# Kernel optimization log

Measured on AMD Instinct MI355X. Metric: run time of the kernel, lower is better.

Reference implementation:

```python
import jax, jax.numpy as jnp
import numpy as np

IN_FEATURES = 1024
OUT_FEATURES = 64   # per-head dim
NUM_HEADS = 16
DIM_PER_HEAD = IN_FEATURES // NUM_HEADS  # used for the 1/sqrt scale, per original code
B, S = 4, 1024


def setup_inputs() -> dict:
    key = jax.random.key(0)
    ks = jax.random.split(key, 12)
    HD = NUM_HEADS * OUT_FEATURES
    s = 1.0 / np.sqrt(IN_FEATURES)
    inp = {
        "q": jax.random.normal(ks[0], (B, S, IN_FEATURES), jnp.float32),
        "k": jax.random.normal(ks[1], (B, S, IN_FEATURES), jnp.float32),
        "v": jax.random.normal(ks[2], (B, S, IN_FEATURES), jnp.float32),
        "q_mask": jax.random.randint(ks[3], (B, S, 1), 0, 2).astype(jnp.float32),
        "k_mask": jax.random.randint(ks[4], (B, S, 1), 0, 2).astype(jnp.float32),
        "Wq": jax.random.normal(ks[5], (IN_FEATURES, HD), jnp.float32) * s,
        "bq": jnp.zeros((HD,), jnp.float32),
        "Wk": jax.random.normal(ks[6], (IN_FEATURES, HD), jnp.float32) * s,
        "bk": jnp.zeros((HD,), jnp.float32),
        "Wv": jax.random.normal(ks[7], (IN_FEATURES, HD), jnp.float32) * s,
        "bv": jnp.zeros((HD,), jnp.float32),
        "Wf": jax.random.normal(ks[8], (HD, IN_FEATURES), jnp.float32) * s,
        "bf": jnp.zeros((IN_FEATURES,), jnp.float32),
        "gamma": jnp.ones((IN_FEATURES,), jnp.float32),
        "beta": jnp.zeros((IN_FEATURES,), jnp.float32),
    }
    return inp


def _layer_norm(x, gamma, beta, eps=1e-5):
    mu = jnp.mean(x, axis=-1, keepdims=True)
    var = jnp.var(x, axis=-1, keepdims=True)
    return (x - mu) * jax.lax.rsqrt(var + eps) * gamma + beta


def reference(q, k, v, q_mask, k_mask, Wq, bq, Wk, bk, Wv, bv, Wf, bf, gamma, beta):
    residual = v
    Bs, Sq, _ = q.shape
    H, Do = NUM_HEADS, OUT_FEATURES
    # QKV projections, split heads: [B, H, S, Do]
    qh = (q @ Wq + bq).reshape(Bs, Sq, H, Do).transpose(0, 2, 1, 3)
    kh = (k @ Wk + bk).reshape(Bs, -1, H, Do).transpose(0, 2, 1, 3)
    vh = (v @ Wv + bv).reshape(Bs, -1, H, Do).transpose(0, 2, 1, 3)
    # custom mask: [B, Sq, Sk] via mask matmul, zero entries are invalid
    mask = jnp.einsum('bqm,bkm->bqk', q_mask, k_mask) / 300.0
    maskz = (mask == 0)[:, None, :, :]  # [B,1,Sq,Sk]
    # raw (unscaled) attention logits, returned as second output
    attention = jnp.einsum('bhqd,bhkd->bhqk', qh, kh)
    scores = attention / np.sqrt(DIM_PER_HEAD)
    scores = jnp.where(maskz, -1e9, scores)
    probs = jax.nn.softmax(scores, axis=-1)
    probs = jnp.where(maskz, 0.0, probs)
    context = jnp.einsum('bhqk,bhkd->bhqd', probs, vh)
    context = context.transpose(0, 2, 1, 3).reshape(Bs, Sq, H * Do)
    out = context @ Wf + bf  # dropout is identity (p=0 / eval)
    out = _layer_norm(out + residual, gamma, beta)
    return out, attention
```

## Files before the change

### kernel.cpp

```cpp
#include <hip/hip_runtime.h>
#include <hip/hip_bf16.h>
#include <stdint.h>


typedef __attribute__((ext_vector_type(8))) short v8s;
typedef __attribute__((ext_vector_type(4))) short v4s;
typedef __attribute__((ext_vector_type(4))) float v4f;

#define S_ 1024
#define MTOT 4096
#define LDA 72
#define LDP 136

#define GLD16(gp, lp)                                                              \
  __builtin_amdgcn_global_load_lds(                                                \
      (const __attribute__((address_space(1))) unsigned int*)(gp),                 \
      (__attribute__((address_space(3))) unsigned int*)(lp), 16, 0, 0)

__device__ __forceinline__ unsigned short f2b(float f) {
  union { float f; unsigned int u; } x; x.f = f;
  unsigned int u = x.u + 0x7fffu + ((x.u >> 16) & 1u);
  return (unsigned short)(u >> 16);
}

__global__ __launch_bounds__(256) void cast3_k(
    const float* __restrict__ q, const float* __restrict__ k, const float* __restrict__ v,
    unsigned short* __restrict__ qb, unsigned short* __restrict__ kb, unsigned short* __restrict__ vb) {
  const float* src = blockIdx.y == 0 ? q : blockIdx.y == 1 ? k : v;
  unsigned short* dst = blockIdx.y == 0 ? qb : blockIdx.y == 1 ? kb : vb;
  int i = (blockIdx.x * 256 + threadIdx.x) * 8;
  v4f a = *(const v4f*)(src + i);
  v4f b = *(const v4f*)(src + i + 4);
  union { unsigned short u[8]; v8s v; } o;
  o.u[0] = f2b(a[0]); o.u[1] = f2b(a[1]); o.u[2] = f2b(a[2]); o.u[3] = f2b(a[3]);
  o.u[4] = f2b(b[0]); o.u[5] = f2b(b[1]); o.u[6] = f2b(b[2]); o.u[7] = f2b(b[3]);
  *(v8s*)(dst + i) = o.v;
}

__global__ __launch_bounds__(256) void transpose_cast_k(
    const float* __restrict__ W0, const float* __restrict__ W1,
    const float* __restrict__ W2, const float* __restrict__ W3,
    unsigned short* __restrict__ T0, unsigned short* __restrict__ T1,
    unsigned short* __restrict__ T2, unsigned short* __restrict__ T3) {
  const float* W = blockIdx.z == 0 ? W0 : blockIdx.z == 1 ? W1 : blockIdx.z == 2 ? W2 : W3;
  unsigned short* T = blockIdx.z == 0 ? T0 : blockIdx.z == 1 ? T1 : blockIdx.z == 2 ? T2 : T3;
  __shared__ float tile[32][33];
  int tx = threadIdx.x & 31, ty = threadIdx.x >> 5;
  int n0 = blockIdx.x * 32, k0 = blockIdx.y * 32;
#pragma unroll
  for (int i = 0; i < 4; i++)
    tile[ty + i * 8][tx] = W[(size_t)(k0 + ty + i * 8) * 1024 + n0 + tx];
  __syncthreads();
#pragma unroll
  for (int i = 0; i < 4; i++)
    T[(size_t)(n0 + ty + i * 8) * 1024 + k0 + tx] = f2b(tile[tx][ty + i * 8]);
}

__global__ __launch_bounds__(256, 2) void qkv_gemm_k(
    const unsigned short* __restrict__ qb, const unsigned short* __restrict__ kb,
    const unsigned short* __restrict__ vb,
    const unsigned short* __restrict__ WqT, const unsigned short* __restrict__ WkT,
    const unsigned short* __restrict__ WvT,
    const float* __restrict__ bq, const float* __restrict__ bk, const float* __restrict__ bv,
    unsigned short* __restrict__ Qh, unsigned short* __restrict__ Kh,
    unsigned short* __restrict__ Vt) {
  __shared__ __align__(16) unsigned short As[128 * 64];
  __shared__ __align__(16) unsigned short Bs[128 * 64];
  const int z = blockIdx.z;
  const unsigned short* A  = z == 0 ? qb : z == 1 ? kb : vb;
  const unsigned short* Bt = z == 0 ? WqT : z == 1 ? WkT : WvT;
  const float* bias        = z == 0 ? bq : z == 1 ? bk : bv;
  unsigned short* Out      = z == 0 ? Qh : z == 1 ? Kh : Vt;
  const int t = threadIdx.x;
  const int wid = t >> 6, lane = t & 63;
  const int lrow = lane & 15, lquad = lane >> 4;
  const int m0 = blockIdx.x * 128, n0 = blockIdx.y * 128;
  const int wm = (wid & 1) * 64, wn = (wid >> 1) * 64;
  v4f zero = {0.f, 0.f, 0.f, 0.f};
  v4f acc[4][4];
#pragma unroll
  for (int i = 0; i < 4; i++)
#pragma unroll
    for (int j = 0; j < 4; j++) acc[i][j] = zero;

  for (int kt = 0; kt < 1024; kt += 64) {
    __syncthreads();
#pragma unroll
    for (int i = 0; i < 4; i++) {
      int c = t + i * 256;
      int r = c >> 3, col8 = (c & 7) * 8;
      GLD16(&A[(size_t)(m0 + r) * 1024 + kt + col8], &As[c * 8]);
      GLD16(&Bt[(size_t)(n0 + r) * 1024 + kt + col8], &Bs[c * 8]);
    }
    __syncthreads();
#pragma unroll
    for (int k32 = 0; k32 < 64; k32 += 32) {
      v8s af[4], bfv[4];
#pragma unroll
      for (int mi = 0; mi < 4; mi++)
        af[mi] = *(const v8s*)&As[(wm + mi * 16 + lrow) * 64 + k32 + lquad * 8];
#pragma unroll
      for (int ni = 0; ni < 4; ni++)
        bfv[ni] = *(const v8s*)&Bs[(wn + ni * 16 + lrow) * 64 + k32 + lquad * 8];
#pragma unroll
      for (int mi = 0; mi < 4; mi++)
#pragma unroll
        for (int ni = 0; ni < 4; ni++)
          acc[mi][ni] = __builtin_amdgcn_mfma_f32_16x16x32_bf16(af[mi], bfv[ni], acc[mi][ni], 0, 0, 0);
    }
  }
#pragma unroll
  for (int mi = 0; mi < 4; mi++) {
#pragma unroll
    for (int ni = 0; ni < 4; ni++) {
      int gn = n0 + wn + ni * 16 + lrow;
      float bv_ = bias[gn];
#pragma unroll
      for (int r = 0; r < 4; r++) {
        int gm = m0 + wm + mi * 16 + lquad * 4 + r;
        float val = acc[mi][ni][r] + bv_;
        int b = gm >> 10, s = gm & 1023, h = gn >> 6, d = gn & 63;
        if (z < 2)
          Out[(size_t)((b * 16 + h) * 1024 + s) * 64 + d] = f2b(val);
        else
          Out[(size_t)((b * 16 + h) * 64 + d) * 1024 + s] = f2b(val);
      }
    }
  }
}

__global__ __launch_bounds__(256, 2) void fgemm_k(
    const unsigned short* __restrict__ A, const unsigned short* __restrict__ Bt,
    float* __restrict__ tmp0, float* __restrict__ tmp1) {
  __shared__ __align__(16) unsigned short As[128 * 64];
  __shared__ __align__(16) unsigned short Bs[128 * 64];
  const int z = blockIdx.z;
  float* Out = z == 0 ? tmp0 : tmp1;
  const int t = threadIdx.x;
  const int wid = t >> 6, lane = t & 63;
  const int lrow = lane & 15, lquad = lane >> 4;
  const int m0 = blockIdx.x * 128, n0 = blockIdx.y * 128;
  const int wm = (wid & 1) * 64, wn = (wid >> 1) * 64;
  v4f zero = {0.f, 0.f, 0.f, 0.f};
  v4f acc[4][4];
#pragma unroll
  for (int i = 0; i < 4; i++)
#pragma unroll
    for (int j = 0; j < 4; j++) acc[i][j] = zero;

  for (int kt = z * 512; kt < z * 512 + 512; kt += 64) {
    __syncthreads();
#pragma unroll
    for (int i = 0; i < 4; i++) {
      int c = t + i * 256;
      int r = c >> 3, col8 = (c & 7) * 8;
      GLD16(&A[(size_t)(m0 + r) * 1024 + kt + col8], &As[c * 8]);
      GLD16(&Bt[(size_t)(n0 + r) * 1024 + kt + col8], &Bs[c * 8]);
    }
    __syncthreads();
#pragma unroll
    for (int k32 = 0; k32 < 64; k32 += 32) {
      v8s af[4], bfv[4];
#pragma unroll
      for (int mi = 0; mi < 4; mi++)
        af[mi] = *(const v8s*)&As[(wm + mi * 16 + lrow) * 64 + k32 + lquad * 8];
#pragma unroll
      for (int ni = 0; ni < 4; ni++)
        bfv[ni] = *(const v8s*)&Bs[(wn + ni * 16 + lrow) * 64 + k32 + lquad * 8];
#pragma unroll
      for (int mi = 0; mi < 4; mi++)
#pragma unroll
        for (int ni = 0; ni < 4; ni++)
          acc[mi][ni] = __builtin_amdgcn_mfma_f32_16x16x32_bf16(af[mi], bfv[ni], acc[mi][ni], 0, 0, 0);
    }
  }
#pragma unroll
  for (int mi = 0; mi < 4; mi++)
#pragma unroll
    for (int ni = 0; ni < 4; ni++) {
      int gn = n0 + wn + ni * 16 + lrow;
#pragma unroll
      for (int r = 0; r < 4; r++) {
        int gm = m0 + wm + mi * 16 + lquad * 4 + r;
        Out[(size_t)gm * 1024 + gn] = acc[mi][ni][r];
      }
    }
}

__global__ __launch_bounds__(256, 2) void attn_fused_k(
    const unsigned short* __restrict__ Qh, const unsigned short* __restrict__ Kh,
    const unsigned short* __restrict__ Vt,
    const float* __restrict__ q_mask, const float* __restrict__ k_mask,
    float* __restrict__ attn, unsigned short* __restrict__ ctx) {
  __shared__ __align__(16) unsigned short Ks[128 * LDA];
  __shared__ __align__(16) unsigned short Pl[4 * 32 * LDP];
  __shared__ __align__(16) float Sl[4 * 32];
  const int z = blockIdx.x, b = z >> 4, h = z & 15;
  const int q0 = blockIdx.y * 128;
  const int t = threadIdx.x, w = t >> 6, lane = t & 63;
  const int lrow = lane & 15, lq = lane >> 4;
  const unsigned short* Kz = Kh + (size_t)z * 1024 * 64;
  const unsigned short* Vz = Vt + (size_t)z * 64 * 1024;
  const float* km = k_mask + b * 1024;
  float* orow = attn + (size_t)z * 1024 * 1024;

  v8s qf[2][2];
#pragma unroll
  for (int ni = 0; ni < 2; ni++)
#pragma unroll
    for (int kb = 0; kb < 2; kb++)
      qf[ni][kb] = *(const v8s*)&Qh[((size_t)z * 1024 + q0 + w * 32 + ni * 16 + lrow) * 64 + kb * 32 + lq * 8];

  v4f zero = {0.f, 0.f, 0.f, 0.f};
  v4f acc_c[2][4];
#pragma unroll
  for (int i = 0; i < 2; i++)
#pragma unroll
    for (int j = 0; j < 4; j++) acc_c[i][j] = zero;
  float m_run[2] = {-1e30f, -1e30f};
  float l_run[2] = {0.f, 0.f};

  for (int kt = 0; kt < 8; kt++) {
    __syncthreads();
#pragma unroll
    for (int i = 0; i < 4; i++) {
      int c = t + i * 256, r = c >> 3, col8 = (c & 7) * 8;
      *(v8s*)&Ks[r * LDA + col8] = *(const v8s*)&Kz[(size_t)(kt * 128 + r) * 64 + col8];
    }
    __syncthreads();
    v4f sa[8][2];
#pragma unroll
    for (int mi = 0; mi < 8; mi++)
#pragma unroll
      for (int ni = 0; ni < 2; ni++) sa[mi][ni] = zero;
#pragma unroll
    for (int kb = 0; kb < 2; kb++) {
      v8s kf[8];
#pragma unroll
      for (int mi = 0; mi < 8; mi++)
        kf[mi] = *(const v8s*)&Ks[(mi * 16 + lrow) * LDA + kb * 32 + lq * 8];
#pragma unroll
      for (int mi = 0; mi < 8; mi++)
#pragma unroll
        for (int ni = 0; ni < 2; ni++)
          sa[mi][ni] = __builtin_amdgcn_mfma_f32_16x16x32_bf16(kf[mi], qf[ni][kb], sa[mi][ni], 0, 0, 0);
    }
#pragma unroll
    for (int mi = 0; mi < 8; mi++)
#pragma unroll
      for (int ni = 0; ni < 2; ni++)
        *(v4f*)&orow[(size_t)(q0 + w * 32 + ni * 16 + lrow) * 1024 + kt * 128 + mi * 16 + lq * 4] = sa[mi][ni];
    int msk[8];
#pragma unroll
    for (int mi = 0; mi < 8; mi++) {
      v4f kv = *(const v4f*)&km[kt * 128 + mi * 16 + lq * 4];
      msk[mi] = (kv[0] != 0.f ? 1 : 0) | (kv[1] != 0.f ? 2 : 0) |
                (kv[2] != 0.f ? 4 : 0) | (kv[3] != 0.f ? 8 : 0);
    }
#pragma unroll
    for (int ni = 0; ni < 2; ni++) {
      float tmax = -1e30f;
#pragma unroll
      for (int mi = 0; mi < 8; mi++)
#pragma unroll
        for (int r = 0; r < 4; r++)
          if ((msk[mi] >> r) & 1) tmax = fmaxf(tmax, sa[mi][ni][r] * 0.125f);
      tmax = fmaxf(tmax, __shfl_xor(tmax, 16));
      tmax = fmaxf(tmax, __shfl_xor(tmax, 32));
      float mnew = fmaxf(m_run[ni], tmax);
      float tsum = 0.f;
#pragma unroll
      for (int mi = 0; mi < 8; mi++) {
        v4s pk;
#pragma unroll
        for (int r = 0; r < 4; r++) {
          float p = ((msk[mi] >> r) & 1) ? __expf(sa[mi][ni][r] * 0.125f - mnew) : 0.f;
          pk[r] = (short)f2b(p);
          tsum += p;
        }
        *(v4s*)&Pl[(w * 32 + ni * 16 + lrow) * LDP + mi * 16 + lq * 4] = pk;
      }
      tsum += __shfl_xor(tsum, 16);
      tsum += __shfl_xor(tsum, 32);
      float sc = __expf(m_run[ni] - mnew);
      l_run[ni] = l_run[ni] * sc + tsum;
      m_run[ni] = mnew;
      if (lq == 0) Sl[w * 32 + ni * 16 + lrow] = sc;
    }
    asm volatile("s_waitcnt lgkmcnt(0)" ::: "memory");
    v4f sc0 = *(const v4f*)&Sl[w * 32 + lq * 4];
    v4f sc1 = *(const v4f*)&Sl[w * 32 + 16 + lq * 4];
#pragma unroll
    for (int nd = 0; nd < 4; nd++)
#pragma unroll
      for (int r = 0; r < 4; r++) {
        acc_c[0][nd][r] *= sc0[r];
        acc_c[1][nd][r] *= sc1[r];
      }
#pragma unroll
    for (int kk = 0; kk < 4; kk++) {
      v8s pa0 = *(const v8s*)&Pl[(w * 32 + lrow) * LDP + kk * 32 + lq * 8];
      v8s pa1 = *(const v8s*)&Pl[(w * 32 + 16 + lrow) * LDP + kk * 32 + lq * 8];
#pragma unroll
      for (int nd = 0; nd < 4; nd++) {
        v8s vb = *(const v8s*)&Vz[(size_t)(nd * 16 + lrow) * 1024 + kt * 128 + kk * 32 + lq * 8];
        acc_c[0][nd] = __builtin_amdgcn_mfma_f32_16x16x32_bf16(pa0, vb, acc_c[0][nd], 0, 0, 0);
        acc_c[1][nd] = __builtin_amdgcn_mfma_f32_16x16x32_bf16(pa1, vb, acc_c[1][nd], 0, 0, 0);
      }
    }
  }
  float qm0 = q_mask[b * 1024 + q0 + w * 32 + lrow];
  float qm1 = q_mask[b * 1024 + q0 + w * 32 + 16 + lrow];
  float r0 = (m_run[0] > -1e29f && l_run[0] > 0.f && qm0 != 0.f) ? (1.f / l_run[0]) : 0.f;
  float r1 = (m_run[1] > -1e29f && l_run[1] > 0.f && qm1 != 0.f) ? (1.f / l_run[1]) : 0.f;
  if (lq == 0) {
    Sl[w * 32 + lrow] = r0;
    Sl[w * 32 + 16 + lrow] = r1;
  }
  asm volatile("s_waitcnt lgkmcnt(0)" ::: "memory");
  v4f rc0 = *(const v4f*)&Sl[w * 32 + lq * 4];
  v4f rc1 = *(const v4f*)&Sl[w * 32 + 16 + lq * 4];
#pragma unroll
  for (int miq = 0; miq < 2; miq++)
#pragma unroll
    for (int nd = 0; nd < 4; nd++)
#pragma unroll
      for (int r = 0; r < 4; r++) {
        int s = q0 + w * 32 + miq * 16 + lq * 4 + r;
        int d = nd * 16 + lrow;
        float rr = (miq == 0) ? rc0[r] : rc1[r];
        ctx[((size_t)(b * 1024 + s)) * 1024 + h * 64 + d] = f2b(acc_c[miq][nd][r] * rr);
      }
}

__global__ __launch_bounds__(256) void resid_ln_k(
    const float* __restrict__ tmp0, const float* __restrict__ tmp1,
    const float* __restrict__ bf, const float* __restrict__ resid,
    const float* __restrict__ gamma, const float* __restrict__ beta,
    float* __restrict__ out) {
  const int r = blockIdx.x, t = threadIdx.x;
  v4f x0 = *(const v4f*)(tmp0 + (size_t)r * 1024 + t * 4);
  v4f x1 = *(const v4f*)(tmp1 + (size_t)r * 1024 + t * 4);
  v4f bv = *(const v4f*)(bf + t * 4);
  v4f rv = *(const v4f*)(resid + (size_t)r * 1024 + t * 4);
  v4f x = x0 + x1 + bv + rv;
  float s = x[0] + x[1] + x[2] + x[3];
  float ss = x[0] * x[0] + x[1] * x[1] + x[2] * x[2] + x[3] * x[3];
#pragma unroll
  for (int off = 32; off; off >>= 1) { s += __shfl_xor(s, off); ss += __shfl_xor(ss, off); }
  __shared__ float red[8];
  const int wid = t >> 6, lane = t & 63;
  if (lane == 0) { red[wid] = s; red[4 + wid] = ss; }
  __syncthreads();
  s = red[0] + red[1] + red[2] + red[3];
  ss = red[4] + red[5] + red[6] + red[7];
  const float mu = s * (1.f / 1024.f);
  float var = ss * (1.f / 1024.f) - mu * mu;
  var = fmaxf(var, 0.f);
  const float rs = rsqrtf(var + 1e-5f);
  v4f g = *(const v4f*)(gamma + t * 4);
  v4f be = *(const v4f*)(beta + t * 4);
  v4f o = (x - mu) * rs * g + be;
  *(v4f*)(out + (size_t)r * 1024 + t * 4) = o;
}

extern "C" void kernel_launch(void* const* d_in, const int* in_sizes, int n_in,
                              void* d_out, int out_size, void* d_ws, size_t ws_size,
                              hipStream_t stream) {
  const float* q      = (const float*)d_in[0];
  const float* k      = (const float*)d_in[1];
  const float* v      = (const float*)d_in[2];
  const float* q_mask = (const float*)d_in[3];
  const float* k_mask = (const float*)d_in[4];
  const float* Wq = (const float*)d_in[5];
  const float* bq = (const float*)d_in[6];
  const float* Wk = (const float*)d_in[7];
  const float* bk = (const float*)d_in[8];
  const float* Wv = (const float*)d_in[9];
  const float* bv = (const float*)d_in[10];
  const float* Wf = (const float*)d_in[11];
  const float* bf = (const float*)d_in[12];
  const float* gamma = (const float*)d_in[13];
  const float* beta  = (const float*)d_in[14];

  float* out0 = (float*)d_out;
  float* attn = out0 + (size_t)MTOT * 1024;

  char* w = (char*)d_ws;
  const size_t MB = (size_t)1 << 20;
  unsigned short* qb  = (unsigned short*)(w + 0);
  unsigned short* kb  = (unsigned short*)(w + 8 * MB);
  unsigned short* vb  = (unsigned short*)(w + 16 * MB);
  unsigned short* WqT = (unsigned short*)(w + 24 * MB);
  unsigned short* WkT = (unsigned short*)(w + 26 * MB);
  unsigned short* WvT = (unsigned short*)(w + 28 * MB);
  unsigned short* WfT = (unsigned short*)(w + 30 * MB);
  unsigned short* Qh  = (unsigned short*)(w + 32 * MB);
  unsigned short* Kh  = (unsigned short*)(w + 40 * MB);
  unsigned short* Vt  = (unsigned short*)(w + 48 * MB);
  unsigned short* ctx = (unsigned short*)(w + 0);
  float* tmp0         = (float*)(w + 8 * MB);
  float* tmp1         = (float*)(w + 32 * MB);

  cast3_k<<<dim3(2048, 3), 256, 0, stream>>>(q, k, v, qb, kb, vb);
  transpose_cast_k<<<dim3(32, 32, 4), 256, 0, stream>>>(Wq, Wk, Wv, Wf, WqT, WkT, WvT, WfT);
  qkv_gemm_k<<<dim3(32, 8, 3), 256, 0, stream>>>(qb, kb, vb, WqT, WkT, WvT, bq, bk, bv, Qh, Kh, Vt);
  attn_fused_k<<<dim3(64, 8), 256, 0, stream>>>(Qh, Kh, Vt, q_mask, k_mask, attn, ctx);
  fgemm_k<<<dim3(32, 8, 2), 256, 0, stream>>>(ctx, WfT, tmp0, tmp1);
  resid_ln_k<<<4096, 256, 0, stream>>>(tmp0, tmp1, bf, v, gamma, beta, out0);
}
```

Before: 482.8 us.

## Double-buffer K tiles via async LDS loads, merge prep kernels, nontemporal attn stores

In the attention kernel, K tiles are now staged with global_load_lds into two XOR-swizzled LDS buffers, and the next tile is prefetched while the current one is computed. This replaces the synchronous padded copy and removes one barrier per iteration. The raw attention logits are written with nontemporal stores to limit cache pollution. The two preprocessing kernels are merged into one launch, and the GEMM launch bounds are raised to 3 blocks per CU. The risks are register pressure from the higher occupancy target and subtle ordering, since a wait on the async loads relies on the barrier placement.

```diff
diff --git a/kernel.cpp b/kernel.cpp
--- a/kernel.cpp
+++ b/kernel.cpp
@@ -9,7 +9,6 @@
 
 #define S_ 1024
 #define MTOT 4096
-#define LDA 72
 #define LDP 136
 
 #define GLD16(gp, lp)                                                              \
@@ -23,40 +22,44 @@
   return (unsigned short)(u >> 16);
 }
 
-__global__ __launch_bounds__(256) void cast3_k(
+__global__ __launch_bounds__(256) void prep_k(
     const float* __restrict__ q, const float* __restrict__ k, const float* __restrict__ v,
-    unsigned short* __restrict__ qb, unsigned short* __restrict__ kb, unsigned short* __restrict__ vb) {
-  const float* src = blockIdx.y == 0 ? q : blockIdx.y == 1 ? k : v;
-  unsigned short* dst = blockIdx.y == 0 ? qb : blockIdx.y == 1 ? kb : vb;
-  int i = (blockIdx.x * 256 + threadIdx.x) * 8;
-  v4f a = *(const v4f*)(src + i);
-  v4f b = *(const v4f*)(src + i + 4);
-  union { unsigned short u[8]; v8s v; } o;
-  o.u[0] = f2b(a[0]); o.u[1] = f2b(a[1]); o.u[2] = f2b(a[2]); o.u[3] = f2b(a[3]);
-  o.u[4] = f2b(b[0]); o.u[5] = f2b(b[1]); o.u[6] = f2b(b[2]); o.u[7] = f2b(b[3]);
-  *(v8s*)(dst + i) = o.v;
-}
-
-__global__ __launch_bounds__(256) void transpose_cast_k(
+    unsigned short* __restrict__ qb, unsigned short* __restrict__ kb, unsigned short* __restrict__ vb,
     const float* __restrict__ W0, const float* __restrict__ W1,
     const float* __restrict__ W2, const float* __restrict__ W3,
     unsigned short* __restrict__ T0, unsigned short* __restrict__ T1,
     unsigned short* __restrict__ T2, unsigned short* __restrict__ T3) {
-  const float* W = blockIdx.z == 0 ? W0 : blockIdx.z == 1 ? W1 : blockIdx.z == 2 ? W2 : W3;
-  unsigned short* T = blockIdx.z == 0 ? T0 : blockIdx.z == 1 ? T1 : blockIdx.z == 2 ? T2 : T3;
-  __shared__ float tile[32][33];
-  int tx = threadIdx.x & 31, ty = threadIdx.x >> 5;
-  int n0 = blockIdx.x * 32, k0 = blockIdx.y * 32;
-#pragma unroll
-  for (int i = 0; i < 4; i++)
-    tile[ty + i * 8][tx] = W[(size_t)(k0 + ty + i * 8) * 1024 + n0 + tx];
-  __syncthreads();
-#pragma unroll
-  for (int i = 0; i < 4; i++)
-    T[(size_t)(n0 + ty + i * 8) * 1024 + k0 + tx] = f2b(tile[tx][ty + i * 8]);
-}
-
-__global__ __launch_bounds__(256, 2) void qkv_gemm_k(
+  const int bid = blockIdx.x;
+  if (bid < 6144) {
+    const int which = bid >> 11;
+    const float* src = which == 0 ? q : which == 1 ? k : v;
+    unsigned short* dst = which == 0 ? qb : which == 1 ? kb : vb;
+    int i = ((bid & 2047) * 256 + threadIdx.x) * 8;
+    v4f a = *(const v4f*)(src + i);
+    v4f b = *(const v4f*)(src + i + 4);
+    union { unsigned short u[8]; v8s v; } o;
+    o.u[0] = f2b(a[0]); o.u[1] = f2b(a[1]); o.u[2] = f2b(a[2]); o.u[3] = f2b(a[3]);
+    o.u[4] = f2b(b[0]); o.u[5] = f2b(b[1]); o.u[6] = f2b(b[2]); o.u[7] = f2b(b[3]);
+    *(v8s*)(dst + i) = o.v;
+  } else {
+    const int bid2 = bid - 6144;
+    const int zz = bid2 >> 10, rem = bid2 & 1023;
+    const float* W = zz == 0 ? W0 : zz == 1 ? W1 : zz == 2 ? W2 : W3;
+    unsigned short* T = zz == 0 ? T0 : zz == 1 ? T1 : zz == 2 ? T2 : T3;
+    __shared__ float tile[32][33];
+    int tx = threadIdx.x & 31, ty = threadIdx.x >> 5;
+    int n0 = (rem & 31) * 32, k0 = (rem >> 5) * 32;
+#pragma unroll
+    for (int i = 0; i < 4; i++)
+      tile[ty + i * 8][tx] = W[(size_t)(k0 + ty + i * 8) * 1024 + n0 + tx];
+    __syncthreads();
+#pragma unroll
+    for (int i = 0; i < 4; i++)
+      T[(size_t)(n0 + ty + i * 8) * 1024 + k0 + tx] = f2b(tile[tx][ty + i * 8]);
+  }
+}
+
+__global__ __launch_bounds__(256, 3) void qkv_gemm_k(
     const unsigned short* __restrict__ qb, const unsigned short* __restrict__ kb,
     const unsigned short* __restrict__ vb,
     const unsigned short* __restrict__ WqT, const unsigned short* __restrict__ WkT,
@@ -129,7 +132,7 @@
   }
 }
 
-__global__ __launch_bounds__(256, 2) void fgemm_k(
+__global__ __launch_bounds__(256, 3) void fgemm_k(
     const unsigned short* __restrict__ A, const unsigned short* __restrict__ Bt,
     float* __restrict__ tmp0, float* __restrict__ tmp1) {
   __shared__ __align__(16) unsigned short As[128 * 64];
@@ -192,7 +195,7 @@
     const unsigned short* __restrict__ Vt,
     const float* __restrict__ q_mask, const float* __restrict__ k_mask,
     float* __restrict__ attn, unsigned short* __restrict__ ctx) {
-  __shared__ __align__(16) unsigned short Ks[128 * LDA];
+  __shared__ __align__(16) unsigned short Ks[2][128 * 64];
   __shared__ __align__(16) unsigned short Pl[4 * 32 * LDP];
   __shared__ __align__(16) float Sl[4 * 32];
   const int z = blockIdx.x, b = z >> 4, h = z & 15;
@@ -204,6 +207,18 @@
   const float* km = k_mask + b * 1024;
   float* orow = attn + (size_t)z * 1024 * 1024;
 
+#define STAGE_K(KT, BUF)                                                            \
+  {                                                                                 \
+    _Pragma("unroll")                                                               \
+    for (int i_ = 0; i_ < 4; i_++) {                                                \
+      int c_ = t + i_ * 256, r_ = c_ >> 3, ch_ = c_ & 7;                            \
+      GLD16(&Kz[(size_t)((KT) * 128 + r_) * 64 + ((ch_ ^ (r_ & 7)) * 8)],           \
+            &Ks[BUF][c_ * 8]);                                                      \
+    }                                                                               \
+  }
+
+  STAGE_K(0, 0);
+
   v8s qf[2][2];
 #pragma unroll
   for (int ni = 0; ni < 2; ni++)
@@ -220,14 +235,11 @@
   float m_run[2] = {-1e30f, -1e30f};
   float l_run[2] = {0.f, 0.f};
 
+  __syncthreads();
+
   for (int kt = 0; kt < 8; kt++) {
-    __syncthreads();
-#pragma unroll
-    for (int i = 0; i < 4; i++) {
-      int c = t + i * 256, r = c >> 3, col8 = (c & 7) * 8;
-      *(v8s*)&Ks[r * LDA + col8] = *(const v8s*)&Kz[(size_t)(kt * 128 + r) * 64 + col8];
-    }
-    __syncthreads();
+    const int cur = kt & 1;
+    if (kt < 7) STAGE_K(kt + 1, cur ^ 1);
     v4f sa[8][2];
 #pragma unroll
     for (int mi = 0; mi < 8; mi++)
@@ -235,10 +247,11 @@
       for (int ni = 0; ni < 2; ni++) sa[mi][ni] = zero;
 #pragma unroll
     for (int kb = 0; kb < 2; kb++) {
+      const int so = ((kb * 4 + lq) ^ (lrow & 7)) * 8;
       v8s kf[8];
 #pragma unroll
       for (int mi = 0; mi < 8; mi++)
-        kf[mi] = *(const v8s*)&Ks[(mi * 16 + lrow) * LDA + kb * 32 + lq * 8];
+        kf[mi] = *(const v8s*)&Ks[cur][(mi * 16 + lrow) * 64 + so];
 #pragma unroll
       for (int mi = 0; mi < 8; mi++)
 #pragma unroll
@@ -249,7 +262,8 @@
     for (int mi = 0; mi < 8; mi++)
 #pragma unroll
       for (int ni = 0; ni < 2; ni++)
-        *(v4f*)&orow[(size_t)(q0 + w * 32 + ni * 16 + lrow) * 1024 + kt * 128 + mi * 16 + lq * 4] = sa[mi][ni];
+        __builtin_nontemporal_store(sa[mi][ni],
+            (v4f*)&orow[(size_t)(q0 + w * 32 + ni * 16 + lrow) * 1024 + kt * 128 + mi * 16 + lq * 4]);
     int msk[8];
 #pragma unroll
     for (int mi = 0; mi < 8; mi++) {
@@ -308,6 +322,7 @@
         acc_c[1][nd] = __builtin_amdgcn_mfma_f32_16x16x32_bf16(pa1, vb, acc_c[1][nd], 0, 0, 0);
       }
     }
+    __syncthreads();
   }
   float qm0 = q_mask[b * 1024 + q0 + w * 32 + lrow];
   float qm1 = q_mask[b * 1024 + q0 + w * 32 + 16 + lrow];
@@ -402,8 +417,7 @@
   float* tmp0         = (float*)(w + 8 * MB);
   float* tmp1         = (float*)(w + 32 * MB);
 
-  cast3_k<<<dim3(2048, 3), 256, 0, stream>>>(q, k, v, qb, kb, vb);
-  transpose_cast_k<<<dim3(32, 32, 4), 256, 0, stream>>>(Wq, Wk, Wv, Wf, WqT, WkT, WvT, WfT);
+  prep_k<<<10240, 256, 0, stream>>>(q, k, v, qb, kb, vb, Wq, Wk, Wv, Wf, WqT, WkT, WvT, WfT);
   qkv_gemm_k<<<dim3(32, 8, 3), 256, 0, stream>>>(qb, kb, vb, WqT, WkT, WvT, bq, bk, bv, Qh, Kh, Vt);
   attn_fused_k<<<dim3(64, 8), 256, 0, stream>>>(Qh, Kh, Vt, q_mask, k_mask, attn, ctx);
   fgemm_k<<<dim3(32, 8, 2), 256, 0, stream>>>(ctx, WfT, tmp0, tmp1);
```

Result: slower. 500.4 us (+3.6%).
